# Performance work log

Hardware: AMD Instinct MI355X
Metric: run time of the kernel (lower is better)

Reference implementation:

```python
import jax, jax.numpy as jnp
import numpy as np
from jax import lax

# Rotation permutations for a flattened 3x3 kernel (row-major, new_flat[t] = orig_flat[perm[t]]),
# transcribed literally from _rotate_kernel for n = angle//45 in {0,1,2,3}.
PERMS = np.array([
    [0, 1, 2, 3, 4, 5, 6, 7, 8],  # 0 deg (identity)
    [3, 0, 1, 6, 4, 2, 7, 8, 5],  # 45 deg: outer ring shifted one step
    [6, 3, 0, 7, 4, 1, 8, 5, 2],  # 90 deg clockwise
    [7, 6, 3, 8, 4, 0, 5, 2, 1],  # 135 deg
], dtype=np.int32)


def setup_inputs() -> dict:
    key = jax.random.key(0)
    k1, k2, k3 = jax.random.split(key, 3)
    B, Cin, Cout, H, W = 16, 64, 64, 128, 128
    x = jax.random.normal(k1, (B, Cin, H, W), dtype=jnp.float32)
    weight = jax.random.normal(k2, (Cout, Cin, 3, 3), dtype=jnp.float32)
    bias = jax.random.normal(k3, (Cout, 1, 1), dtype=jnp.float32)
    return {"x": x, "weight": weight, "bias": bias}


def reference(x, weight, bias):
    # x: [B, Cin, H, W]; weight: [Cout, Cin, 3, 3]; bias: [Cout, 1, 1]
    B, Cin, H, W = x.shape
    Cout = weight.shape[0]
    n_ang = PERMS.shape[0]

    # Build the 4 rotated kernel variants in one gather.
    wflat = weight.reshape(Cout, Cin, 9)
    # [Cout, Cin, n_ang, 9] -> [n_ang, Cout, Cin, 3, 3] -> merge angle into output channels
    wrot = wflat[:, :, jnp.asarray(PERMS)].transpose(2, 0, 1, 3).reshape(n_ang * Cout, Cin, 3, 3)

    # ZeroPad2d(stride=1) then valid 3x3 conv -> same spatial size.
    xp = jnp.pad(x, ((0, 0), (0, 0), (1, 1), (1, 1)))
    y = lax.conv_general_dilated(
        xp, wrot, window_strides=(1, 1), padding="VALID",
        dimension_numbers=("NCHW", "OIHW", "NCHW"))  # [B, n_ang*Cout, H, W]

    y = y.reshape(B, n_ang, Cout, H, W).transpose(1, 0, 2, 3, 4)  # [n_ang, B, Cout, H, W]
    return y + bias  # bias (Cout,1,1) broadcasts over trailing dims
```

## Files before the change

kernel.cpp:

```cpp
#include <hip/hip_runtime.h>


#define CIN 64
#define COUT 64
#define HH 128
#define WW 128
#define NB 16
#define HW (HH*WW)

typedef short bf16x8 __attribute__((ext_vector_type(8)));
typedef float f32x16 __attribute__((ext_vector_type(16)));

#define XS_SLOT 1072
#define XS_ROW  8576
#define XS_OFF  73728
#define LDS_BYTES (XS_OFF + 4 * XS_ROW)

__device__ __constant__ unsigned char DHI_d[4][9] = {
  {0,0,0,1,1,1,2,2,2},
  {0,0,1,0,1,2,1,2,2},
  {0,1,2,0,1,2,0,1,2},
  {1,2,2,0,1,2,0,0,1},
};
__device__ __constant__ unsigned short DWB_d[4][9] = {
  {0,16,32,0,16,32,0,16,32},
  {16,32,32,0,16,32,0,0,16},
  {32,32,32,16,16,16,0,0,0},
  {32,32,16,32,16,0,16,0,0},
};

static __device__ __forceinline__ unsigned short f2bf(float f) {
  unsigned u = __builtin_bit_cast(unsigned, f);
  return (unsigned short)((u + 0x7FFFu + ((u >> 16) & 1u)) >> 16);
}
static __device__ __forceinline__ unsigned pk2(float lo, float hi) {
  return (unsigned)f2bf(lo) | ((unsigned)f2bf(hi) << 16);
}

__global__ void build_A_kernel(const float* __restrict__ wgt,
                               unsigned short* __restrict__ A) {
  const int e = blockIdx.x * 256 + threadIdx.x;
  const int j = e & 7;
  const int cm = (e >> 3) & 63;
  const int half = (e >> 9) & 1;
  const int kc = e >> 10;
  const int s = kc >> 2, q = kc & 3;
  const int ci = q * 16 + half * 8 + j;
  A[e] = f2bf(wgt[(cm * CIN + ci) * 9 + s]);
}

static __device__ __forceinline__ void lgkm_barrier() {
  asm volatile("s_waitcnt lgkmcnt(0)" ::: "memory");
  __builtin_amdgcn_s_barrier();
}

__global__ __launch_bounds__(512) void aconv_v7_kernel(
    const float* __restrict__ x,
    const unsigned short* __restrict__ Ag,
    const float* __restrict__ bias,
    float* __restrict__ out)
{
  __shared__ __align__(16) unsigned char lds[LDS_BYTES];

  const int tid = threadIdx.x;
  const int lane = tid & 63;
  const int wid = tid >> 6;
  const int a   = wid >> 1;
  const int row = wid & 1;
  const int half = lane >> 5;
  const int ln = lane & 31;

  const int blk = blockIdx.x;
  const int b   = blk >> 4;
  const int rem = blk & 15;
  const int hbase = rem * 8;

  float bv[2][16];
  #pragma unroll
  for (int mf = 0; mf < 2; ++mf)
    #pragma unroll
    for (int g = 0; g < 16; ++g)
      bv[mf][g] = bias[mf * 32 + (g & 3) + 8 * (g >> 2) + 4 * half];

  int dhi[9]; unsigned dwb[9];
  #pragma unroll
  for (int s = 0; s < 9; ++s) { dhi[s] = DHI_d[a][s]; dwb[s] = DWB_d[a][s]; }

  {
    const uint4* Ag4 = (const uint4*)Ag;
    uint4* As4 = (uint4*)lds;
    #pragma unroll
    for (int i = 0; i < 9; ++i) As4[tid + i * 512] = Ag4[tid + i * 512];
  }

  float gv[5][8];
  unsigned gdst[5];
  bool gval[5];

  #pragma unroll
  for (int i = 0; i < 5; ++i) {
    const int g = tid + i * 512;
    const bool v = g < 2112;
    const int rg = g / 528;
    const int rest = g - rg * 528;
    const int slot = rest / 66;
    const int wI = rest - slot * 66;
    const int hx = hbase - 1 + rg;
    const int gw = -1 + wI;
    const bool inb = v && ((unsigned)hx < HH) && ((unsigned)gw < WW);
    const float* xp = x + (size_t)(b * CIN + slot * 8) * HW + (size_t)hx * WW + gw;
    gval[i] = v;
    gdst[i] = (unsigned)(XS_OFF + rg * XS_ROW + slot * XS_SLOT + wI * 16);
    #pragma unroll
    for (int q = 0; q < 8; ++q) gv[i][q] = inb ? xp[(size_t)q * HW] : 0.f;
  }
  #pragma unroll
  for (int i = 0; i < 5; ++i)
    if (gval[i]) {
      uint4 u;
      u.x = pk2(gv[i][0], gv[i][1]); u.y = pk2(gv[i][2], gv[i][3]);
      u.z = pk2(gv[i][4], gv[i][5]); u.w = pk2(gv[i][6], gv[i][7]);
      *(uint4*)(lds + gdst[i]) = u;
    }
  __syncthreads();

  const unsigned char* Asb = lds + (unsigned)(half * 1024 + ln * 16);
  const unsigned char* Bsb = lds + XS_OFF + (unsigned)(half * XS_SLOT + ln * 16);

  #pragma unroll 1
  for (int ti = 0; ti < 8; ++ti) {
    const int wh = ti >> 2, it = ti & 3;
    const int w0 = wh * 64;

    unsigned boff_t[9];
    {
      unsigned rowoff[3];
      #pragma unroll
      for (int dh = 0; dh < 3; ++dh)
        rowoff[dh] = (unsigned)(((2 * it + row + dh) & 3) * XS_ROW);
      #pragma unroll
      for (int s = 0; s < 9; ++s) boff_t[s] = dwb[s] + rowoff[dhi[s]];
    }

    const bool pf2 = (it < 3);
    const bool pf4 = (it == 3) && (wh == 0);
    const int ngran = pf2 ? 1056 : (pf4 ? 2112 : 0);
    if (ngran) {
      const int itv = pf4 ? -2 : it;
      const int w0n = pf4 ? 64 : w0;
      #pragma unroll
      for (int i = 0; i < 5; ++i) {
        const int g = tid + i * 512;
        const bool v = g < ngran;
        const int rg = g / 528;
        const int rest = g - rg * 528;
        const int slot = rest / 66;
        const int wI = rest - slot * 66;
        const int hx = hbase + 2 * itv + 3 + rg;
        const int ps = (2 * itv + 4 + rg) & 3;
        const int gw = w0n - 1 + wI;
        const bool inb = v && ((unsigned)hx < HH) && ((unsigned)gw < WW);
        const float* xp = x + (size_t)(b * CIN + slot * 8) * HW + (size_t)hx * WW + gw;
        gval[i] = v;
        gdst[i] = (unsigned)(XS_OFF + ps * XS_ROW + slot * XS_SLOT + wI * 16);
        #pragma unroll
        for (int q = 0; q < 8; ++q) gv[i][q] = inb ? xp[(size_t)q * HW] : 0.f;
      }
    }

    f32x16 acc[2][2];
    #pragma unroll
    for (int mf = 0; mf < 2; ++mf)
      #pragma unroll
      for (int nf = 0; nf < 2; ++nf)
        #pragma unroll
        for (int g = 0; g < 16; ++g)
          acc[mf][nf][g] = bv[mf][g];

    #pragma unroll
    for (int kc = 0; kc < 36; ++kc) {
      const bf16x8 af0 = *(const bf16x8*)(Asb + kc * 2048);
      const bf16x8 af1 = *(const bf16x8*)(Asb + kc * 2048 + 512);
      const unsigned bb = boff_t[kc >> 2] + (unsigned)((kc & 3) * 2 * XS_SLOT);
      const bf16x8 bf0 = *(const bf16x8*)(Bsb + bb);
      const bf16x8 bf1 = *(const bf16x8*)(Bsb + bb + 512);
      acc[0][0] = __builtin_amdgcn_mfma_f32_32x32x16_bf16(af0, bf0, acc[0][0], 0, 0, 0);
      acc[0][1] = __builtin_amdgcn_mfma_f32_32x32x16_bf16(af0, bf1, acc[0][1], 0, 0, 0);
      acc[1][0] = __builtin_amdgcn_mfma_f32_32x32x16_bf16(af1, bf0, acc[1][0], 0, 0, 0);
      acc[1][1] = __builtin_amdgcn_mfma_f32_32x32x16_bf16(af1, bf1, acc[1][1], 0, 0, 0);
    }

    const int hout = hbase + it * 2 + row;
    #pragma unroll
    for (int mf = 0; mf < 2; ++mf)
      #pragma unroll
      for (int nf = 0; nf < 2; ++nf) {
        const f32x16 v = acc[mf][nf];
        float* op = out + (((size_t)(a * NB + b) * COUT + mf * 32 + 4 * half) * HH
                           + hout) * WW + w0 + nf * 32 + ln;
        #pragma unroll
        for (int g = 0; g < 16; ++g)
          __builtin_nontemporal_store(v[g], op + (size_t)((g & 3) + 8 * (g >> 2)) * HW);
      }

    lgkm_barrier();
    if (ngran) {
      #pragma unroll
      for (int i = 0; i < 5; ++i)
        if (gval[i]) {
          uint4 u;
          u.x = pk2(gv[i][0], gv[i][1]); u.y = pk2(gv[i][2], gv[i][3]);
          u.z = pk2(gv[i][4], gv[i][5]); u.w = pk2(gv[i][6], gv[i][7]);
          *(uint4*)(lds + gdst[i]) = u;
        }
    }
    lgkm_barrier();
  }
}

extern "C" void kernel_launch(void* const* d_in, const int* in_sizes, int n_in,
                              void* d_out, int out_size, void* d_ws, size_t ws_size,
                              hipStream_t stream) {
  const float* x    = (const float*)d_in[0];
  const float* wgt  = (const float*)d_in[1];
  const float* bias = (const float*)d_in[2];
  float* out = (float*)d_out;
  unsigned short* A = (unsigned short*)d_ws;

  build_A_kernel<<<144, 256, 0, stream>>>(wgt, A);
  aconv_v7_kernel<<<256, 512, 0, stream>>>(x, A, bias, out);
}
```

Measured before the change: 101.3 us.

## Use 1024-thread blocks covering full row width and fold bias into an MFMA

Each block now has 16 waves, with the two 64-column halves of a row handled by separate waves at the same time instead of in a sequential loop. The LDS input staging is changed to hold the full 130-column width, and each thread loads a single column so the gather addressing is simpler. Bias now enters through an extra K-step: a bias row is appended to the A matrix, multiplied by a ones vector, and no longer needs per-lane bias registers. Packing of prefetched rows is moved to the middle of the MFMA loop so it can overlap with the matrix work. The cost is higher register and LDS pressure per block and one extra MFMA step per tile.

```diff
diff --git a/kernel.cpp b/kernel.cpp
--- a/kernel.cpp
+++ b/kernel.cpp
@@ -11,9 +11,9 @@
 typedef short bf16x8 __attribute__((ext_vector_type(8)));
 typedef float f32x16 __attribute__((ext_vector_type(16)));
 
-#define XS_SLOT 1072
-#define XS_ROW  8576
-#define XS_OFF  73728
+#define XS_SLOT 2080
+#define XS_ROW  16640
+#define XS_OFF  75776
 #define LDS_BYTES (XS_OFF + 4 * XS_ROW)
 
 __device__ __constant__ unsigned char DHI_d[4][9] = {
@@ -38,15 +38,20 @@
 }
 
 __global__ void build_A_kernel(const float* __restrict__ wgt,
+                               const float* __restrict__ bias,
                                unsigned short* __restrict__ A) {
   const int e = blockIdx.x * 256 + threadIdx.x;
   const int j = e & 7;
   const int cm = (e >> 3) & 63;
   const int half = (e >> 9) & 1;
   const int kc = e >> 10;
-  const int s = kc >> 2, q = kc & 3;
-  const int ci = q * 16 + half * 8 + j;
-  A[e] = f2bf(wgt[(cm * CIN + ci) * 9 + s]);
+  if (kc < 36) {
+    const int s = kc >> 2, q = kc & 3;
+    const int ci = q * 16 + half * 8 + j;
+    A[e] = f2bf(wgt[(cm * CIN + ci) * 9 + s]);
+  } else {
+    A[e] = (half == 0 && j == 0) ? f2bf(bias[cm]) : (unsigned short)0;
+  }
 }
 
 static __device__ __forceinline__ void lgkm_barrier() {
@@ -54,10 +59,9 @@
   __builtin_amdgcn_s_barrier();
 }
 
-__global__ __launch_bounds__(512) void aconv_v7_kernel(
+__global__ __launch_bounds__(1024) void aconv_v8_kernel(
     const float* __restrict__ x,
     const unsigned short* __restrict__ Ag,
-    const float* __restrict__ bias,
     float* __restrict__ out)
 {
   __shared__ __align__(16) unsigned char lds[LDS_BYTES];
@@ -65,8 +69,9 @@
   const int tid = threadIdx.x;
   const int lane = tid & 63;
   const int wid = tid >> 6;
-  const int a   = wid >> 1;
-  const int row = wid & 1;
+  const int a   = wid >> 2;
+  const int row = (wid >> 1) & 1;
+  const int wh  = wid & 1;
   const int half = lane >> 5;
   const int ln = lane & 31;
 
@@ -75,13 +80,6 @@
   const int rem = blk & 15;
   const int hbase = rem * 8;
 
-  float bv[2][16];
-  #pragma unroll
-  for (int mf = 0; mf < 2; ++mf)
-    #pragma unroll
-    for (int g = 0; g < 16; ++g)
-      bv[mf][g] = bias[mf * 32 + (g & 3) + 8 * (g >> 2) + 4 * half];
-
   int dhi[9]; unsigned dwb[9];
   #pragma unroll
   for (int s = 0; s < 9; ++s) { dhi[s] = DHI_d[a][s]; dwb[s] = DWB_d[a][s]; }
@@ -90,81 +88,71 @@
     const uint4* Ag4 = (const uint4*)Ag;
     uint4* As4 = (uint4*)lds;
     #pragma unroll
-    for (int i = 0; i < 9; ++i) As4[tid + i * 512] = Ag4[tid + i * 512];
-  }
-
-  float gv[5][8];
-  unsigned gdst[5];
-  bool gval[5];
-
-  #pragma unroll
-  for (int i = 0; i < 5; ++i) {
-    const int g = tid + i * 512;
-    const bool v = g < 2112;
-    const int rg = g / 528;
-    const int rest = g - rg * 528;
-    const int slot = rest / 66;
-    const int wI = rest - slot * 66;
-    const int hx = hbase - 1 + rg;
-    const int gw = -1 + wI;
-    const bool inb = v && ((unsigned)hx < HH) && ((unsigned)gw < WW);
-    const float* xp = x + (size_t)(b * CIN + slot * 8) * HW + (size_t)hx * WW + gw;
-    gval[i] = v;
-    gdst[i] = (unsigned)(XS_OFF + rg * XS_ROW + slot * XS_SLOT + wI * 16);
-    #pragma unroll
-    for (int q = 0; q < 8; ++q) gv[i][q] = inb ? xp[(size_t)q * HW] : 0.f;
-  }
-  #pragma unroll
-  for (int i = 0; i < 5; ++i)
-    if (gval[i]) {
+    for (int i = 0; i < 5; ++i) {
+      const int g = tid + i * 1024;
+      if (g < 4736) As4[g] = Ag4[g];
+    }
+  }
+  if (tid < 64) {
+    const int rs = tid >> 4, cs = (tid >> 1) & 7, side = tid & 1;
+    uint4 z = {0u, 0u, 0u, 0u};
+    *(uint4*)(lds + XS_OFF + rs * XS_ROW + cs * XS_SLOT + side * 129 * 16) = z;
+  }
+
+  const int scs = (tid >> 7) & 7;
+  const int swc = tid & 127;
+  const float* sxb = x + (size_t)(b * CIN + scs * 8) * HW + swc;
+  const unsigned sdstb = (unsigned)(XS_OFF + scs * XS_SLOT + (1 + swc) * 16);
+
+  {
+    float pv[4][8];
+    #pragma unroll
+    for (int rr = 0; rr < 4; ++rr) {
+      const int gh = hbase - 1 + rr;
+      const bool inb = (unsigned)gh < HH;
+      const float* xp = sxb + (size_t)gh * WW;
+      #pragma unroll
+      for (int q = 0; q < 8; ++q) pv[rr][q] = inb ? xp[(size_t)q * HW] : 0.f;
+    }
+    #pragma unroll
+    for (int rr = 0; rr < 4; ++rr) {
       uint4 u;
-      u.x = pk2(gv[i][0], gv[i][1]); u.y = pk2(gv[i][2], gv[i][3]);
-      u.z = pk2(gv[i][4], gv[i][5]); u.w = pk2(gv[i][6], gv[i][7]);
-      *(uint4*)(lds + gdst[i]) = u;
-    }
+      u.x = pk2(pv[rr][0], pv[rr][1]); u.y = pk2(pv[rr][2], pv[rr][3]);
+      u.z = pk2(pv[rr][4], pv[rr][5]); u.w = pk2(pv[rr][6], pv[rr][7]);
+      *(uint4*)(lds + sdstb + rr * XS_ROW) = u;
+    }
+  }
   __syncthreads();
 
   const unsigned char* Asb = lds + (unsigned)(half * 1024 + ln * 16);
-  const unsigned char* Bsb = lds + XS_OFF + (unsigned)(half * XS_SLOT + ln * 16);
+  const unsigned char* Bsb = lds + XS_OFF + (unsigned)(half * XS_SLOT + (wh * 64 + ln) * 16);
+
+  bf16x8 ob = (bf16x8)(short)0;
+  if (half == 0) ob[0] = (short)0x3F80;
 
   #pragma unroll 1
-  for (int ti = 0; ti < 8; ++ti) {
-    const int wh = ti >> 2, it = ti & 3;
-    const int w0 = wh * 64;
+  for (int it = 0; it < 4; ++it) {
+    const bool pf = (it < 3);
 
     unsigned boff_t[9];
     {
       unsigned rowoff[3];
       #pragma unroll
       for (int dh = 0; dh < 3; ++dh)
-        rowoff[dh] = (unsigned)(((2 * it + row + dh) & 3) * XS_ROW);
+        rowoff[dh] = (unsigned)(((it * 2 + row + dh) & 3) * XS_ROW);
       #pragma unroll
       for (int s = 0; s < 9; ++s) boff_t[s] = dwb[s] + rowoff[dhi[s]];
     }
 
-    const bool pf2 = (it < 3);
-    const bool pf4 = (it == 3) && (wh == 0);
-    const int ngran = pf2 ? 1056 : (pf4 ? 2112 : 0);
-    if (ngran) {
-      const int itv = pf4 ? -2 : it;
-      const int w0n = pf4 ? 64 : w0;
-      #pragma unroll
-      for (int i = 0; i < 5; ++i) {
-        const int g = tid + i * 512;
-        const bool v = g < ngran;
-        const int rg = g / 528;
-        const int rest = g - rg * 528;
-        const int slot = rest / 66;
-        const int wI = rest - slot * 66;
-        const int hx = hbase + 2 * itv + 3 + rg;
-        const int ps = (2 * itv + 4 + rg) & 3;
-        const int gw = w0n - 1 + wI;
-        const bool inb = v && ((unsigned)hx < HH) && ((unsigned)gw < WW);
-        const float* xp = x + (size_t)(b * CIN + slot * 8) * HW + (size_t)hx * WW + gw;
-        gval[i] = v;
-        gdst[i] = (unsigned)(XS_OFF + ps * XS_ROW + slot * XS_SLOT + wI * 16);
+    float gv[2][8];
+    if (pf) {
+      #pragma unroll
+      for (int rr = 0; rr < 2; ++rr) {
+        const int gh = hbase + it * 2 + 3 + rr;
+        const bool inb = (unsigned)gh < HH;
+        const float* xp = sxb + (size_t)gh * WW;
         #pragma unroll
-        for (int q = 0; q < 8; ++q) gv[i][q] = inb ? xp[(size_t)q * HW] : 0.f;
+        for (int q = 0; q < 8; ++q) gv[rr][q] = inb ? xp[(size_t)q * HW] : 0.f;
       }
     }
 
@@ -172,13 +160,9 @@
     #pragma unroll
     for (int mf = 0; mf < 2; ++mf)
       #pragma unroll
-      for (int nf = 0; nf < 2; ++nf)
-        #pragma unroll
-        for (int g = 0; g < 16; ++g)
-          acc[mf][nf][g] = bv[mf][g];
-
-    #pragma unroll
-    for (int kc = 0; kc < 36; ++kc) {
+      for (int nf = 0; nf < 2; ++nf) acc[mf][nf] = (f32x16)(0.f);
+
+    auto kstep = [&](int kc) {
       const bf16x8 af0 = *(const bf16x8*)(Asb + kc * 2048);
       const bf16x8 af1 = *(const bf16x8*)(Asb + kc * 2048 + 512);
       const unsigned bb = boff_t[kc >> 2] + (unsigned)((kc & 3) * 2 * XS_SLOT);
@@ -188,6 +172,30 @@
       acc[0][1] = __builtin_amdgcn_mfma_f32_32x32x16_bf16(af0, bf1, acc[0][1], 0, 0, 0);
       acc[1][0] = __builtin_amdgcn_mfma_f32_32x32x16_bf16(af1, bf0, acc[1][0], 0, 0, 0);
       acc[1][1] = __builtin_amdgcn_mfma_f32_32x32x16_bf16(af1, bf1, acc[1][1], 0, 0, 0);
+    };
+
+    #pragma unroll
+    for (int kc = 0; kc < 18; ++kc) kstep(kc);
+
+    uint4 gp[2];
+    if (pf) {
+      #pragma unroll
+      for (int rr = 0; rr < 2; ++rr) {
+        gp[rr].x = pk2(gv[rr][0], gv[rr][1]); gp[rr].y = pk2(gv[rr][2], gv[rr][3]);
+        gp[rr].z = pk2(gv[rr][4], gv[rr][5]); gp[rr].w = pk2(gv[rr][6], gv[rr][7]);
+      }
+    }
+
+    #pragma unroll
+    for (int kc = 18; kc < 36; ++kc) kstep(kc);
+
+    {
+      const bf16x8 af0 = *(const bf16x8*)(Asb + 36 * 2048);
+      const bf16x8 af1 = *(const bf16x8*)(Asb + 36 * 2048 + 512);
+      acc[0][0] = __builtin_amdgcn_mfma_f32_32x32x16_bf16(af0, ob, acc[0][0], 0, 0, 0);
+      acc[0][1] = __builtin_amdgcn_mfma_f32_32x32x16_bf16(af0, ob, acc[0][1], 0, 0, 0);
+      acc[1][0] = __builtin_amdgcn_mfma_f32_32x32x16_bf16(af1, ob, acc[1][0], 0, 0, 0);
+      acc[1][1] = __builtin_amdgcn_mfma_f32_32x32x16_bf16(af1, ob, acc[1][1], 0, 0, 0);
     }
 
     const int hout = hbase + it * 2 + row;
@@ -197,22 +205,19 @@
       for (int nf = 0; nf < 2; ++nf) {
         const f32x16 v = acc[mf][nf];
         float* op = out + (((size_t)(a * NB + b) * COUT + mf * 32 + 4 * half) * HH
-                           + hout) * WW + w0 + nf * 32 + ln;
+                           + hout) * WW + wh * 64 + nf * 32 + ln;
         #pragma unroll
         for (int g = 0; g < 16; ++g)
           __builtin_nontemporal_store(v[g], op + (size_t)((g & 3) + 8 * (g >> 2)) * HW);
       }
 
     lgkm_barrier();
-    if (ngran) {
-      #pragma unroll
-      for (int i = 0; i < 5; ++i)
-        if (gval[i]) {
-          uint4 u;
-          u.x = pk2(gv[i][0], gv[i][1]); u.y = pk2(gv[i][2], gv[i][3]);
-          u.z = pk2(gv[i][4], gv[i][5]); u.w = pk2(gv[i][6], gv[i][7]);
-          *(uint4*)(lds + gdst[i]) = u;
-        }
+    if (pf) {
+      #pragma unroll
+      for (int rr = 0; rr < 2; ++rr) {
+        const unsigned slot = (unsigned)((it * 2 + 4 + rr) & 3);
+        *(uint4*)(lds + sdstb + slot * XS_ROW) = gp[rr];
+      }
     }
     lgkm_barrier();
   }
@@ -227,6 +232,6 @@
   float* out = (float*)d_out;
   unsigned short* A = (unsigned short*)d_ws;
 
-  build_A_kernel<<<144, 256, 0, stream>>>(wgt, A);
-  aconv_v7_kernel<<<256, 512, 0, stream>>>(x, A, bias, out);
-}
+  build_A_kernel<<<148, 256, 0, stream>>>(wgt, bias, A);
+  aconv_v8_kernel<<<256, 1024, 0, stream>>>(x, A, out);
+}
```

New measurement: 114.3 us. 1.13x slower.

## Pre-pack input to bf16 channel-interleaved layout and stream tiles via global_load_lds

Applied to the files above, without the earlier changes.

Adds a pre-pass that converts x to bf16 in a channel-interleaved [B,H,slot,W] layout in workspace. A new conv kernel with 1024 threads covers the full 128-wide row per block and loads input rows and weights straight into LDS with global_load_lds, so the per-element fp32 gathers and in-register packing go away. Bias is folded in as an extra MFMA k-step against a ones vector instead of initialising the accumulators. The cost is an extra full pass over x plus workspace traffic, and a larger block that may limit occupancy. The old kernel is kept as a fallback when workspace is too small.

```diff
diff --git a/kernel.cpp b/kernel.cpp
--- a/kernel.cpp
+++ b/kernel.cpp
@@ -10,11 +10,8 @@
 
 typedef short bf16x8 __attribute__((ext_vector_type(8)));
 typedef float f32x16 __attribute__((ext_vector_type(16)));
-
-#define XS_SLOT 1072
-#define XS_ROW  8576
-#define XS_OFF  73728
-#define LDS_BYTES (XS_OFF + 4 * XS_ROW)
+#define AS1 __attribute__((address_space(1)))
+#define AS3 __attribute__((address_space(3)))
 
 __device__ __constant__ unsigned char DHI_d[4][9] = {
   {0,0,0,1,1,1,2,2,2},
@@ -37,17 +34,185 @@
   return (unsigned)f2bf(lo) | ((unsigned)f2bf(hi) << 16);
 }
 
+__global__ __launch_bounds__(256) void xt_build_kernel(const float* __restrict__ x,
+                                                       unsigned short* __restrict__ xt) {
+  const int gid = blockIdx.x * 256 + threadIdx.x;
+  const int w = gid & 127;
+  const int h = (gid >> 7) & 127;
+  const int slot = (gid >> 14) & 7;
+  const int b = gid >> 17;
+  const float* xp = x + ((size_t)(b * CIN + slot * 8) * HH + h) * WW + w;
+  uint4 u;
+  u.x = pk2(xp[0], xp[HW]);
+  u.y = pk2(xp[2 * HW], xp[3 * HW]);
+  u.z = pk2(xp[4 * HW], xp[5 * HW]);
+  u.w = pk2(xp[6 * HW], xp[7 * HW]);
+  const size_t idx = ((size_t)(b * HH + h) * 8 + slot) * 128 + w;
+  *(uint4*)((unsigned char*)xt + idx * 16) = u;
+}
+
 __global__ void build_A_kernel(const float* __restrict__ wgt,
+                               const float* __restrict__ bias,
                                unsigned short* __restrict__ A) {
   const int e = blockIdx.x * 256 + threadIdx.x;
   const int j = e & 7;
   const int cm = (e >> 3) & 63;
   const int half = (e >> 9) & 1;
   const int kc = e >> 10;
-  const int s = kc >> 2, q = kc & 3;
-  const int ci = q * 16 + half * 8 + j;
-  A[e] = f2bf(wgt[(cm * CIN + ci) * 9 + s]);
-}
+  if (kc < 36) {
+    const int s = kc >> 2, q = kc & 3;
+    const int ci = q * 16 + half * 8 + j;
+    A[e] = f2bf(wgt[(cm * CIN + ci) * 9 + s]);
+  } else if (kc == 36) {
+    A[e] = (half == 0 && j == 0) ? f2bf(bias[cm]) : (unsigned short)0;
+  }
+}
+
+#define V9_SLOT 2080
+#define V9_ROW  16640
+#define V9_XOFF 75776
+#define V9_LDS  (V9_XOFF + 4 * V9_ROW)
+
+__global__ __launch_bounds__(1024, 4) void aconv_v9_kernel(
+    const unsigned short* __restrict__ xt,
+    const unsigned short* __restrict__ Ag,
+    float* __restrict__ out)
+{
+  __shared__ __align__(16) unsigned char lds[V9_LDS];
+
+  const int tid = threadIdx.x;
+  const int lane = tid & 63;
+  const int wid = tid >> 6;
+  const int a   = wid >> 2;
+  const int row = (wid >> 1) & 1;
+  const int wh  = wid & 1;
+  const int half = lane >> 5;
+  const int ln = lane & 31;
+
+  const int b   = blockIdx.x >> 4;
+  const int rem = blockIdx.x & 15;
+  const int hbase = rem * 8;
+
+  const unsigned char* Agb = (const unsigned char*)Ag;
+  const unsigned char* xtb = (const unsigned char*)xt;
+  AS3 unsigned char* ldsa = (AS3 unsigned char*)lds;
+  const uint4 z4 = {0u, 0u, 0u, 0u};
+
+  #pragma unroll
+  for (int j = 0; j < 5; ++j) {
+    const int i = wid + j * 16;
+    if (i < 74)
+      __builtin_amdgcn_global_load_lds(
+          (const AS1 unsigned*)(Agb + i * 1024 + lane * 16),
+          (AS3 unsigned*)(ldsa + i * 1024), 16, 0, 0);
+  }
+  if (tid < 64) {
+    const int rs = tid >> 4, cs = (tid >> 1) & 7, side = tid & 1;
+    *(uint4*)(lds + V9_XOFF + rs * V9_ROW + cs * V9_SLOT + side * 129 * 16) = z4;
+  }
+  #pragma unroll
+  for (int j = 0; j < 4; ++j) {
+    const int c = wid + j * 16;
+    const int rr = c >> 4;
+    const int s  = (c >> 1) & 7;
+    const int k  = c & 1;
+    const int gh = hbase - 1 + rr;
+    const unsigned dst = (unsigned)(V9_XOFF + rr * V9_ROW + s * V9_SLOT + 16 + k * 1024);
+    if (gh >= 0) {
+      __builtin_amdgcn_global_load_lds(
+          (const AS1 unsigned*)(xtb + ((size_t)((b * HH + gh) * 8 + s) * 128 + k * 64) * 16 + lane * 16),
+          (AS3 unsigned*)(ldsa + dst), 16, 0, 0);
+    } else {
+      *(uint4*)(lds + dst + lane * 16) = z4;
+    }
+  }
+  __syncthreads();
+
+  const unsigned char* Asb = lds + (unsigned)(half * 1024 + ln * 16);
+  const unsigned char* Bsb = lds + V9_XOFF + (unsigned)(half * V9_SLOT + (wh * 64 + ln) * 16);
+
+  bf16x8 ob = (bf16x8)(short)0;
+  if (half == 0) ob[0] = (short)0x3F80;
+
+  #pragma unroll 1
+  for (int it = 0; it < 4; ++it) {
+    unsigned boff_t[9];
+    #pragma unroll
+    for (int s = 0; s < 9; ++s)
+      boff_t[s] = (unsigned)DWB_d[a][s]
+                + (unsigned)(((it * 2 + row + (int)DHI_d[a][s]) & 3) * V9_ROW);
+
+    f32x16 acc[2][2];
+    #pragma unroll
+    for (int mf = 0; mf < 2; ++mf)
+      #pragma unroll
+      for (int nf = 0; nf < 2; ++nf) acc[mf][nf] = (f32x16)(0.f);
+
+    #pragma unroll
+    for (int kc = 0; kc < 36; ++kc) {
+      const bf16x8 af0 = *(const bf16x8*)(Asb + kc * 2048);
+      const bf16x8 af1 = *(const bf16x8*)(Asb + kc * 2048 + 512);
+      const unsigned bb = boff_t[kc >> 2] + (unsigned)((kc & 3) * 2 * V9_SLOT);
+      const bf16x8 bf0 = *(const bf16x8*)(Bsb + bb);
+      const bf16x8 bf1 = *(const bf16x8*)(Bsb + bb + 512);
+      acc[0][0] = __builtin_amdgcn_mfma_f32_32x32x16_bf16(af0, bf0, acc[0][0], 0, 0, 0);
+      acc[0][1] = __builtin_amdgcn_mfma_f32_32x32x16_bf16(af0, bf1, acc[0][1], 0, 0, 0);
+      acc[1][0] = __builtin_amdgcn_mfma_f32_32x32x16_bf16(af1, bf0, acc[1][0], 0, 0, 0);
+      acc[1][1] = __builtin_amdgcn_mfma_f32_32x32x16_bf16(af1, bf1, acc[1][1], 0, 0, 0);
+    }
+    {
+      const bf16x8 af0 = *(const bf16x8*)(Asb + 36 * 2048);
+      const bf16x8 af1 = *(const bf16x8*)(Asb + 36 * 2048 + 512);
+      acc[0][0] = __builtin_amdgcn_mfma_f32_32x32x16_bf16(af0, ob, acc[0][0], 0, 0, 0);
+      acc[0][1] = __builtin_amdgcn_mfma_f32_32x32x16_bf16(af0, ob, acc[0][1], 0, 0, 0);
+      acc[1][0] = __builtin_amdgcn_mfma_f32_32x32x16_bf16(af1, ob, acc[1][0], 0, 0, 0);
+      acc[1][1] = __builtin_amdgcn_mfma_f32_32x32x16_bf16(af1, ob, acc[1][1], 0, 0, 0);
+    }
+
+    const int hout = hbase + it * 2 + row;
+    #pragma unroll
+    for (int mf = 0; mf < 2; ++mf)
+      #pragma unroll
+      for (int nf = 0; nf < 2; ++nf) {
+        const f32x16 v = acc[mf][nf];
+        float* op = out + (((size_t)(a * NB + b) * COUT + mf * 32 + 4 * half) * HH
+                           + hout) * WW + wh * 64 + nf * 32 + ln;
+        #pragma unroll
+        for (int g = 0; g < 16; ++g)
+          __builtin_nontemporal_store(v[g], op + (size_t)((g & 3) + 8 * (g >> 2)) * HW);
+      }
+
+    asm volatile("s_waitcnt lgkmcnt(0)" ::: "memory");
+    __builtin_amdgcn_s_barrier();
+
+    if (it < 3) {
+      #pragma unroll
+      for (int j = 0; j < 2; ++j) {
+        const int c = wid + j * 16;
+        const int rr = c >> 4;
+        const int s  = (c >> 1) & 7;
+        const int k  = c & 1;
+        const int gh = hbase + it * 2 + 3 + rr;
+        const unsigned dst = (unsigned)(V9_XOFF + ((it * 2 + rr) & 3) * V9_ROW
+                                        + s * V9_SLOT + 16 + k * 1024);
+        if (gh < HH) {
+          __builtin_amdgcn_global_load_lds(
+              (const AS1 unsigned*)(xtb + ((size_t)((b * HH + gh) * 8 + s) * 128 + k * 64) * 16 + lane * 16),
+              (AS3 unsigned*)(ldsa + dst), 16, 0, 0);
+        } else {
+          *(uint4*)(lds + dst + lane * 16) = z4;
+        }
+      }
+      asm volatile("s_waitcnt vmcnt(0) lgkmcnt(0)" ::: "memory");
+      __builtin_amdgcn_s_barrier();
+    }
+  }
+}
+
+#define R7_SLOT 1072
+#define R7_ROW  8576
+#define R7_XOFF 73728
+#define R7_LDS  (R7_XOFF + 4 * R7_ROW)
 
 static __device__ __forceinline__ void lgkm_barrier() {
   asm volatile("s_waitcnt lgkmcnt(0)" ::: "memory");
@@ -60,7 +225,7 @@
     const float* __restrict__ bias,
     float* __restrict__ out)
 {
-  __shared__ __align__(16) unsigned char lds[LDS_BYTES];
+  __shared__ __align__(16) unsigned char lds[R7_LDS];
 
   const int tid = threadIdx.x;
   const int lane = tid & 63;
@@ -110,7 +275,7 @@
     const bool inb = v && ((unsigned)hx < HH) && ((unsigned)gw < WW);
     const float* xp = x + (size_t)(b * CIN + slot * 8) * HW + (size_t)hx * WW + gw;
     gval[i] = v;
-    gdst[i] = (unsigned)(XS_OFF + rg * XS_ROW + slot * XS_SLOT + wI * 16);
+    gdst[i] = (unsigned)(R7_XOFF + rg * R7_ROW + slot * R7_SLOT + wI * 16);
     #pragma unroll
     for (int q = 0; q < 8; ++q) gv[i][q] = inb ? xp[(size_t)q * HW] : 0.f;
   }
@@ -125,7 +290,7 @@
   __syncthreads();
 
   const unsigned char* Asb = lds + (unsigned)(half * 1024 + ln * 16);
-  const unsigned char* Bsb = lds + XS_OFF + (unsigned)(half * XS_SLOT + ln * 16);
+  const unsigned char* Bsb = lds + R7_XOFF + (unsigned)(half * R7_SLOT + ln * 16);
 
   #pragma unroll 1
   for (int ti = 0; ti < 8; ++ti) {
@@ -137,7 +302,7 @@
       unsigned rowoff[3];
       #pragma unroll
       for (int dh = 0; dh < 3; ++dh)
-        rowoff[dh] = (unsigned)(((2 * it + row + dh) & 3) * XS_ROW);
+        rowoff[dh] = (unsigned)(((2 * it + row + dh) & 3) * R7_ROW);
       #pragma unroll
       for (int s = 0; s < 9; ++s) boff_t[s] = dwb[s] + rowoff[dhi[s]];
     }
@@ -162,7 +327,7 @@
         const bool inb = v && ((unsigned)hx < HH) && ((unsigned)gw < WW);
         const float* xp = x + (size_t)(b * CIN + slot * 8) * HW + (size_t)hx * WW + gw;
         gval[i] = v;
-        gdst[i] = (unsigned)(XS_OFF + ps * XS_ROW + slot * XS_SLOT + wI * 16);
+        gdst[i] = (unsigned)(R7_XOFF + ps * R7_ROW + slot * R7_SLOT + wI * 16);
         #pragma unroll
         for (int q = 0; q < 8; ++q) gv[i][q] = inb ? xp[(size_t)q * HW] : 0.f;
       }
@@ -181,7 +346,7 @@
     for (int kc = 0; kc < 36; ++kc) {
       const bf16x8 af0 = *(const bf16x8*)(Asb + kc * 2048);
       const bf16x8 af1 = *(const bf16x8*)(Asb + kc * 2048 + 512);
-      const unsigned bb = boff_t[kc >> 2] + (unsigned)((kc & 3) * 2 * XS_SLOT);
+      const unsigned bb = boff_t[kc >> 2] + (unsigned)((kc & 3) * 2 * R7_SLOT);
       const bf16x8 bf0 = *(const bf16x8*)(Bsb + bb);
       const bf16x8 bf1 = *(const bf16x8*)(Bsb + bb + 512);
       acc[0][0] = __builtin_amdgcn_mfma_f32_32x32x16_bf16(af0, bf0, acc[0][0], 0, 0, 0);
@@ -225,8 +390,19 @@
   const float* wgt  = (const float*)d_in[1];
   const float* bias = (const float*)d_in[2];
   float* out = (float*)d_out;
-  unsigned short* A = (unsigned short*)d_ws;
-
-  build_A_kernel<<<144, 256, 0, stream>>>(wgt, A);
-  aconv_v7_kernel<<<256, 512, 0, stream>>>(x, A, bias, out);
-}
+
+  const size_t XT_BYTES = (size_t)NB * HH * 8 * 128 * 16;
+  const size_t A_BYTES  = 75776;
+
+  if (ws_size >= XT_BYTES + A_BYTES) {
+    unsigned short* xt = (unsigned short*)d_ws;
+    unsigned short* A  = (unsigned short*)((char*)d_ws + XT_BYTES);
+    build_A_kernel<<<148, 256, 0, stream>>>(wgt, bias, A);
+    xt_build_kernel<<<8192, 256, 0, stream>>>(x, xt);
+    aconv_v9_kernel<<<256, 1024, 0, stream>>>(xt, A, out);
+  } else {
+    unsigned short* A = (unsigned short*)d_ws;
+    build_A_kernel<<<148, 256, 0, stream>>>(wgt, bias, A);
+    aconv_v7_kernel<<<256, 512, 0, stream>>>(x, A, bias, out);
+  }
+}
```

Result: slower. 119.4 us (+17.9%).
